# Kernel optimization log

Measured on AMD Instinct MI355X. Metric: run time of the kernel, lower is better.

Reference implementation:

```python
import jax, jax.numpy as jnp
import numpy as np

Q, C, S, D = 2048, 10, 16, 256
H = [256, 128, 64, 10]

def _init_linear(key, fan_in, fan_out):
    kw, kb = jax.random.split(key)
    bound = 1.0 / np.sqrt(fan_in)
    W = jax.random.uniform(kw, (fan_in, fan_out), jnp.float32, -bound, bound)
    b = jax.random.uniform(kb, (fan_out,), jnp.float32, -bound, bound)
    return W, b

def setup_inputs() -> dict:
    key = jax.random.key(0)
    ks = jax.random.split(key, 6)
    queries = jax.random.normal(ks[0], (Q, D), jnp.float32)
    supports = jax.random.normal(ks[1], (C, S, D), jnp.float32)
    W1, b1 = _init_linear(ks[2], 2 * D, H[0])
    W2, b2 = _init_linear(ks[3], H[0], H[1])
    W3, b3 = _init_linear(ks[4], H[1], H[2])
    W4, b4 = _init_linear(ks[5], H[2], H[3])
    return {"queries": queries, "supports": supports,
            "W1": W1, "b1": b1, "W2": W2, "b2": b2,
            "W3": W3, "b3": b3, "W4": W4, "b4": b4}

def reference(queries, supports, W1, b1, W2, b2, W3, b3, W4, b4):
    # queries: [Q, D]; supports: [C, S, D]
    q, d = queries.shape
    c, s, _ = supports.shape
    # Build all (query, support-item) pairs: [Q, C, S, 2D]
    qb = jnp.broadcast_to(queries[:, None, None, :], (q, c, s, d))
    sb = jnp.broadcast_to(supports[None, :, :, :], (q, c, s, d))
    x = jnp.concatenate([qb, sb], axis=-1)
    h = jax.nn.relu(x @ W1 + b1)
    h = jax.nn.relu(h @ W2 + b2)
    h = jax.nn.relu(h @ W3 + b3)
    out = jnp.tanh(h @ W4 + b4)          # [Q, C, S, 10]
    item_score = out.mean(axis=-1)       # [Q, C, S] (Simnet mean over 10 outputs)
    scores = item_score.sum(axis=-1)     # sum over support items -> [Q, C]
    return scores
```

## Files before the change

kernel.cpp:

```cpp
#include <hip/hip_runtime.h>
#include <hip/hip_bf16.h>
#include <math.h>

#define QN 2048
#define CN 10
#define SN 16
#define DN 256
#define H1N 256
#define H2N 128
#define H3N 64
#define H4N 10
#define NROW 160
#define PRE_AB_BLOCKS (QN / 4 + NROW / 4)

#define S1 528
#define S2 272
#define S3 144

typedef __attribute__((ext_vector_type(8)))  short  bf16x8s;
typedef __attribute__((ext_vector_type(4)))  float  f32x4;
typedef __attribute__((ext_vector_type(16))) float  f32x16;

static __device__ __forceinline__ unsigned short f2bf(float f) {
  __hip_bfloat16 h = __float2bfloat16(f);
  return __builtin_bit_cast(unsigned short, h);
}

static __device__ __forceinline__ float fast_tanh(float x) {
  const float xc = fminf(fmaxf(x, -15.f), 15.f);
  const float e = __expf(2.f * xc);
  return (e - 1.f) / (e + 1.f);
}

__global__ __launch_bounds__(256) void k_pre(
    const float* __restrict__ queries, const float* __restrict__ supports,
    const float* __restrict__ W1, const float* __restrict__ b1,
    const float* __restrict__ W2, const float* __restrict__ W3,
    const float* __restrict__ W4,
    float* __restrict__ A, float* __restrict__ Bm,
    ushort* __restrict__ fb2, ushort* __restrict__ fb3, ushort* __restrict__ fb4) {
  __shared__ float xs[4][DN];
  const int bid = blockIdx.x;
  const int t = threadIdx.x;

  if (bid < PRE_AB_BLOCKS) {
    const bool isA = bid < (QN / 4);
    const int row0 = isA ? bid * 4 : (bid - QN / 4) * 4;
    const float* src = isA ? (queries + (size_t)row0 * DN) : (supports + (size_t)row0 * DN);
    for (int r = 0; r < 4; ++r) xs[r][t] = src[r * DN + t];
    __syncthreads();
    const float* w = W1 + (isA ? 0 : DN * H1N) + t;
    float acc0 = 0.f, acc1 = 0.f, acc2 = 0.f, acc3 = 0.f;
#pragma unroll 8
    for (int d = 0; d < DN; ++d) {
      const float wv = w[(size_t)d * H1N];
      acc0 += xs[0][d] * wv;
      acc1 += xs[1][d] * wv;
      acc2 += xs[2][d] * wv;
      acc3 += xs[3][d] * wv;
    }
    const float bias = isA ? b1[t] : 0.f;
    float* dst = isA ? A : Bm;
    dst[(row0 + 0) * H1N + t] = acc0 + bias;
    dst[(row0 + 1) * H1N + t] = acc1 + bias;
    dst[(row0 + 2) * H1N + t] = acc2 + bias;
    dst[(row0 + 3) * H1N + t] = acc3 + bias;
    return;
  }

  const int f = (bid - PRE_AB_BLOCKS) * 4 + (t >> 6);
  const int l = t & 63;
  if (f >= 82) return;
  ushort o[8];
  if (f < 64) {
    const int ct = f >> 4, ks = f & 15;
    const int col = ct * 32 + (l & 31);
    const int k0 = ks * 16 + (l >> 5) * 8;
#pragma unroll
    for (int j = 0; j < 8; ++j) o[j] = f2bf(W2[(size_t)(k0 + j) * H2N + col]);
#pragma unroll
    for (int j = 0; j < 8; ++j) fb2[(size_t)f * 512 + l * 8 + j] = o[j];
  } else if (f < 80) {
    const int g = f - 64;
    const int ct = g >> 3, ks = g & 7;
    const int col = ct * 32 + (l & 31);
    const int k0 = ks * 16 + (l >> 5) * 8;
#pragma unroll
    for (int j = 0; j < 8; ++j) o[j] = f2bf(W3[(size_t)(k0 + j) * H3N + col]);
#pragma unroll
    for (int j = 0; j < 8; ++j) fb3[(size_t)g * 512 + l * 8 + j] = o[j];
  } else {
    const int ks = f - 80;
    const int col = l & 15;
    const int k0 = ks * 32 + (l >> 4) * 8;
#pragma unroll
    for (int j = 0; j < 8; ++j)
      o[j] = (col < H4N) ? f2bf(W4[(size_t)(k0 + j) * H4N + col]) : (ushort)0;
#pragma unroll
    for (int j = 0; j < 8; ++j) fb4[(size_t)ks * 512 + l * 8 + j] = o[j];
  }
}

__global__ __launch_bounds__(512, 2) void k_main(
    const float* __restrict__ A, const float* __restrict__ Bm,
    const ushort* __restrict__ fb2, const ushort* __restrict__ fb3,
    const ushort* __restrict__ fb4,
    const float* __restrict__ b2, const float* __restrict__ b3,
    const float* __restrict__ b4, float* __restrict__ out) {
  __shared__ __align__(16) unsigned char smem[128 * S1];
  unsigned char* h1s = smem;
  unsigned char* h2s = smem;
  unsigned char* h3s = smem + 128 * S2;

  const int t = threadIdx.x;
  const int wid = t >> 6;
  const int l = t & 63;
  const int l31 = l & 31;
  const int l15 = l & 15;
  const int wr = wid >> 1;
  const int wc = wid & 1;

  const bf16x8s* fb2v = (const bf16x8s*)fb2;
  const bf16x8s* fb3v = (const bf16x8s*)fb3;
  const bf16x8s* fb4v = (const bf16x8s*)fb4;

  bf16x8s B3r[8];
#pragma unroll
  for (int ks = 0; ks < 8; ++ks) B3r[ks] = fb3v[(wc * 8 + ks) * 64 + l];
  const int c0g2 = 64 * wc + l31;
  const float bias2a = b2[c0g2], bias2b = b2[c0g2 + 32];
  const float bias3 = b3[32 * wc + l31];

  const int rg0 = blockIdx.x * 128;
  const int q0 = rg0 / NROW;
  const int b0 = rg0 - q0 * NROW;
#pragma unroll 4
  for (int r = 0; r < 16; ++r) {
    const int row = wid * 16 + r;
    int bb = b0 + row;
    int qq = q0;
    if (bb >= NROW) { bb -= NROW; qq += 1; }
    const float4 av = *(const float4*)(A + (size_t)qq * DN + l * 4);
    const float4 bv = *(const float4*)(Bm + (size_t)bb * DN + l * 4);
    ushort4 o;
    o.x = f2bf(fmaxf(av.x + bv.x, 0.f));
    o.y = f2bf(fmaxf(av.y + bv.y, 0.f));
    o.z = f2bf(fmaxf(av.z + bv.z, 0.f));
    o.w = f2bf(fmaxf(av.w + bv.w, 0.f));
    *(ushort4*)(h1s + row * S1 + l * 8) = o;
  }
  __syncthreads();

  f32x16 acc2a, acc2b;
#pragma unroll
  for (int i = 0; i < 16; ++i) { acc2a[i] = 0.f; acc2b[i] = 0.f; }
  {
    const unsigned char* abase = h1s + (32 * wr + l31) * S1;
    const int kh = (l >> 5) * 16;
    const int ct0 = wc * 2;
    bf16x8s a_cur = *(const bf16x8s*)(abase + kh);
    bf16x8s pA0 = fb2v[((ct0 + 0) * 16 + 0) * 64 + l];
    bf16x8s pB0 = fb2v[((ct0 + 1) * 16 + 0) * 64 + l];
    bf16x8s pA1 = fb2v[((ct0 + 0) * 16 + 1) * 64 + l];
    bf16x8s pB1 = fb2v[((ct0 + 1) * 16 + 1) * 64 + l];
#pragma unroll
    for (int ks = 0; ks < 16; ++ks) {
      const bf16x8s a_use = a_cur;
      const bf16x8s bA = (ks & 1) ? pA1 : pA0;
      const bf16x8s bB = (ks & 1) ? pB1 : pB0;
      if (ks + 1 < 16) a_cur = *(const bf16x8s*)(abase + (ks + 1) * 32 + kh);
      if (ks + 2 < 16) {
        if (ks & 1) {
          pA1 = fb2v[((ct0 + 0) * 16 + ks + 2) * 64 + l];
          pB1 = fb2v[((ct0 + 1) * 16 + ks + 2) * 64 + l];
        } else {
          pA0 = fb2v[((ct0 + 0) * 16 + ks + 2) * 64 + l];
          pB0 = fb2v[((ct0 + 1) * 16 + ks + 2) * 64 + l];
        }
      }
      acc2a = __builtin_amdgcn_mfma_f32_32x32x16_bf16(a_use, bA, acc2a, 0, 0, 0);
      acc2b = __builtin_amdgcn_mfma_f32_32x32x16_bf16(a_use, bB, acc2b, 0, 0, 0);
    }
  }
  __syncthreads();
  {
#pragma unroll
    for (int reg = 0; reg < 16; ++reg) {
      const int row = 32 * wr + (reg & 3) + 8 * (reg >> 2) + 4 * (l >> 5);
      *(ushort*)(h2s + row * S2 + c0g2 * 2) =
          f2bf(fmaxf(acc2a[reg] + bias2a, 0.f));
      *(ushort*)(h2s + row * S2 + c0g2 * 2 + 64) =
          f2bf(fmaxf(acc2b[reg] + bias2b, 0.f));
    }
  }

  bf16x8s B4r[2];
  B4r[0] = fb4v[l];
  B4r[1] = fb4v[64 + l];
  const float b4v = (l15 < H4N) ? b4[l15] : 0.f;
  __syncthreads();

  f32x16 acc3;
#pragma unroll
  for (int i = 0; i < 16; ++i) acc3[i] = 0.f;
  {
    const unsigned char* abase = h2s + (32 * wr + l31) * S2;
    const int kh = (l >> 5) * 16;
    bf16x8s a_cur = *(const bf16x8s*)(abase + kh);
#pragma unroll
    for (int ks = 0; ks < 8; ++ks) {
      const bf16x8s a_use = a_cur;
      if (ks + 1 < 8) a_cur = *(const bf16x8s*)(abase + (ks + 1) * 32 + kh);
      acc3 = __builtin_amdgcn_mfma_f32_32x32x16_bf16(a_use, B3r[ks], acc3, 0, 0, 0);
    }
  }
  {
#pragma unroll
    for (int reg = 0; reg < 16; ++reg) {
      const int row = 32 * wr + (reg & 3) + 8 * (reg >> 2) + 4 * (l >> 5);
      *(ushort*)(h3s + row * S3 + (32 * wc + l31) * 2) =
          f2bf(fmaxf(acc3[reg] + bias3, 0.f));
    }
  }
  __syncthreads();

  f32x4 acc4;
#pragma unroll
  for (int i = 0; i < 4; ++i) acc4[i] = 0.f;
  {
    const unsigned char* abase = h3s + (16 * wid + l15) * S3;
#pragma unroll
    for (int ks = 0; ks < 2; ++ks) {
      const bf16x8s a = *(const bf16x8s*)(abase + (l >> 4) * 16 + ks * 64);
      acc4 = __builtin_amdgcn_mfma_f32_16x16x32_bf16(a, B4r[ks], acc4, 0, 0, 0);
    }
  }

  {
    float part = 0.f;
#pragma unroll
    for (int r = 0; r < 4; ++r) {
      const float v = fast_tanh(acc4[r] + b4v);
      part += (l15 < H4N) ? v : 0.f;
    }
    part += __shfl_xor(part, 1);
    part += __shfl_xor(part, 2);
    part += __shfl_xor(part, 4);
    part += __shfl_xor(part, 8);
    part += __shfl_xor(part, 16);
    part += __shfl_xor(part, 32);
    if (l == 0) out[(size_t)blockIdx.x * 8 + wid] = part * 0.1f;
  }
}

extern "C" void kernel_launch(void* const* d_in, const int* in_sizes, int n_in,
                              void* d_out, int out_size, void* d_ws, size_t ws_size,
                              hipStream_t stream) {
  const float* queries  = (const float*)d_in[0];
  const float* supports = (const float*)d_in[1];
  const float* W1 = (const float*)d_in[2];
  const float* b1 = (const float*)d_in[3];
  const float* W2 = (const float*)d_in[4];
  const float* b2 = (const float*)d_in[5];
  const float* W3 = (const float*)d_in[6];
  const float* b3 = (const float*)d_in[7];
  const float* W4 = (const float*)d_in[8];
  const float* b4 = (const float*)d_in[9];
  float* out = (float*)d_out;

  float* A  = (float*)d_ws;
  float* Bm = A + (size_t)QN * H1N;
  ushort* fb2 = (ushort*)(Bm + (size_t)NROW * H1N);
  ushort* fb3 = fb2 + 64 * 512;
  ushort* fb4 = fb3 + 16 * 512;

  hipLaunchKernelGGL(k_pre, dim3(PRE_AB_BLOCKS + 21), dim3(256), 0, stream,
                     queries, supports, W1, b1, W2, W3, W4, A, Bm, fb2, fb3, fb4);
  hipLaunchKernelGGL(k_main, dim3((QN * CN * SN) / 128), dim3(512), 0, stream,
                     A, Bm, fb2, fb3, fb4, b2, b3, b4, out);
}
```

Before: 74.68 us.

## Split layer-2 K into halves to shrink LDS and raise occupancy

The layer-1 activation tile is now built and consumed in two K-halves of 128 columns through a smaller shared buffer, so LDS per block drops from about 66KB to about 53KB. The launch bound is raised from 2 to 6 blocks per multiprocessor. Manual software prefetching of A and B fragments is removed in favour of direct loads. The goal is to hide latency through higher occupancy, at the cost of extra barriers, register pressure from the tighter launch bound, and less explicit overlap within each wave.

```diff
diff --git a/kernel.cpp b/kernel.cpp
--- a/kernel.cpp
+++ b/kernel.cpp
@@ -13,8 +13,7 @@
 #define NROW 160
 #define PRE_AB_BLOCKS (QN / 4 + NROW / 4)
 
-#define S1 528
-#define S2 272
+#define SH 272
 #define S3 144
 
 typedef __attribute__((ext_vector_type(8)))  short  bf16x8s;
@@ -101,22 +100,23 @@
   }
 }
 
-__global__ __launch_bounds__(512, 2) void k_main(
+__global__ __launch_bounds__(512, 6) void k_main(
     const float* __restrict__ A, const float* __restrict__ Bm,
     const ushort* __restrict__ fb2, const ushort* __restrict__ fb3,
     const ushort* __restrict__ fb4,
     const float* __restrict__ b2, const float* __restrict__ b3,
     const float* __restrict__ b4, float* __restrict__ out) {
-  __shared__ __align__(16) unsigned char smem[128 * S1];
+  __shared__ __align__(16) unsigned char smem[128 * SH + 128 * S3];
   unsigned char* h1s = smem;
   unsigned char* h2s = smem;
-  unsigned char* h3s = smem + 128 * S2;
+  unsigned char* h3s = smem + 128 * SH;
 
   const int t = threadIdx.x;
   const int wid = t >> 6;
   const int l = t & 63;
   const int l31 = l & 31;
   const int l15 = l & 15;
+  const int lh = l >> 5;
   const int wr = wid >> 1;
   const int wc = wid & 1;
 
@@ -134,62 +134,53 @@
   const int rg0 = blockIdx.x * 128;
   const int q0 = rg0 / NROW;
   const int b0 = rg0 - q0 * NROW;
-#pragma unroll 4
-  for (int r = 0; r < 16; ++r) {
-    const int row = wid * 16 + r;
-    int bb = b0 + row;
-    int qq = q0;
-    if (bb >= NROW) { bb -= NROW; qq += 1; }
-    const float4 av = *(const float4*)(A + (size_t)qq * DN + l * 4);
-    const float4 bv = *(const float4*)(Bm + (size_t)bb * DN + l * 4);
-    ushort4 o;
-    o.x = f2bf(fmaxf(av.x + bv.x, 0.f));
-    o.y = f2bf(fmaxf(av.y + bv.y, 0.f));
-    o.z = f2bf(fmaxf(av.z + bv.z, 0.f));
-    o.w = f2bf(fmaxf(av.w + bv.w, 0.f));
-    *(ushort4*)(h1s + row * S1 + l * 8) = o;
-  }
-  __syncthreads();
+  const int ct0 = wc * 2;
+  const unsigned char* abase2 = h1s + (32 * wr + l31) * SH;
+  const int kh = lh * 16;
 
   f32x16 acc2a, acc2b;
 #pragma unroll
   for (int i = 0; i < 16; ++i) { acc2a[i] = 0.f; acc2b[i] = 0.f; }
-  {
-    const unsigned char* abase = h1s + (32 * wr + l31) * S1;
-    const int kh = (l >> 5) * 16;
-    const int ct0 = wc * 2;
-    bf16x8s a_cur = *(const bf16x8s*)(abase + kh);
-    bf16x8s pA0 = fb2v[((ct0 + 0) * 16 + 0) * 64 + l];
-    bf16x8s pB0 = fb2v[((ct0 + 1) * 16 + 0) * 64 + l];
-    bf16x8s pA1 = fb2v[((ct0 + 0) * 16 + 1) * 64 + l];
-    bf16x8s pB1 = fb2v[((ct0 + 1) * 16 + 1) * 64 + l];
-#pragma unroll
-    for (int ks = 0; ks < 16; ++ks) {
-      const bf16x8s a_use = a_cur;
-      const bf16x8s bA = (ks & 1) ? pA1 : pA0;
-      const bf16x8s bB = (ks & 1) ? pB1 : pB0;
-      if (ks + 1 < 16) a_cur = *(const bf16x8s*)(abase + (ks + 1) * 32 + kh);
-      if (ks + 2 < 16) {
-        if (ks & 1) {
-          pA1 = fb2v[((ct0 + 0) * 16 + ks + 2) * 64 + l];
-          pB1 = fb2v[((ct0 + 1) * 16 + ks + 2) * 64 + l];
-        } else {
-          pA0 = fb2v[((ct0 + 0) * 16 + ks + 2) * 64 + l];
-          pB0 = fb2v[((ct0 + 1) * 16 + ks + 2) * 64 + l];
-        }
-      }
-      acc2a = __builtin_amdgcn_mfma_f32_32x32x16_bf16(a_use, bA, acc2a, 0, 0, 0);
-      acc2b = __builtin_amdgcn_mfma_f32_32x32x16_bf16(a_use, bB, acc2b, 0, 0, 0);
-    }
-  }
-  __syncthreads();
+
+#pragma unroll
+  for (int hf = 0; hf < 2; ++hf) {
+#pragma unroll
+    for (int it = 0; it < 8; ++it) {
+      const int row = wid * 16 + it * 2 + lh;
+      int bb = b0 + row;
+      int qq = q0;
+      if (bb >= NROW) { bb -= NROW; qq += 1; }
+      const int col = hf * 128 + l31 * 4;
+      const float4 av = *(const float4*)(A + (size_t)qq * DN + col);
+      const float4 bv = *(const float4*)(Bm + (size_t)bb * DN + col);
+      ushort4 o;
+      o.x = f2bf(fmaxf(av.x + bv.x, 0.f));
+      o.y = f2bf(fmaxf(av.y + bv.y, 0.f));
+      o.z = f2bf(fmaxf(av.z + bv.z, 0.f));
+      o.w = f2bf(fmaxf(av.w + bv.w, 0.f));
+      *(ushort4*)(h1s + row * SH + l31 * 8) = o;
+    }
+    __syncthreads();
+
+#pragma unroll
+    for (int ks = 0; ks < 8; ++ks) {
+      const int ksg = hf * 8 + ks;
+      const bf16x8s a = *(const bf16x8s*)(abase2 + ks * 32 + kh);
+      const bf16x8s bA = fb2v[((ct0 + 0) * 16 + ksg) * 64 + l];
+      const bf16x8s bB = fb2v[((ct0 + 1) * 16 + ksg) * 64 + l];
+      acc2a = __builtin_amdgcn_mfma_f32_32x32x16_bf16(a, bA, acc2a, 0, 0, 0);
+      acc2b = __builtin_amdgcn_mfma_f32_32x32x16_bf16(a, bB, acc2b, 0, 0, 0);
+    }
+    __syncthreads();
+  }
+
   {
 #pragma unroll
     for (int reg = 0; reg < 16; ++reg) {
-      const int row = 32 * wr + (reg & 3) + 8 * (reg >> 2) + 4 * (l >> 5);
-      *(ushort*)(h2s + row * S2 + c0g2 * 2) =
+      const int row = 32 * wr + (reg & 3) + 8 * (reg >> 2) + 4 * lh;
+      *(ushort*)(h2s + row * SH + c0g2 * 2) =
           f2bf(fmaxf(acc2a[reg] + bias2a, 0.f));
-      *(ushort*)(h2s + row * S2 + c0g2 * 2 + 64) =
+      *(ushort*)(h2s + row * SH + c0g2 * 2 + 64) =
           f2bf(fmaxf(acc2b[reg] + bias2b, 0.f));
     }
   }
@@ -204,20 +195,17 @@
 #pragma unroll
   for (int i = 0; i < 16; ++i) acc3[i] = 0.f;
   {
-    const unsigned char* abase = h2s + (32 * wr + l31) * S2;
-    const int kh = (l >> 5) * 16;
-    bf16x8s a_cur = *(const bf16x8s*)(abase + kh);
+    const unsigned char* abase = h2s + (32 * wr + l31) * SH;
 #pragma unroll
     for (int ks = 0; ks < 8; ++ks) {
-      const bf16x8s a_use = a_cur;
-      if (ks + 1 < 8) a_cur = *(const bf16x8s*)(abase + (ks + 1) * 32 + kh);
-      acc3 = __builtin_amdgcn_mfma_f32_32x32x16_bf16(a_use, B3r[ks], acc3, 0, 0, 0);
+      const bf16x8s a = *(const bf16x8s*)(abase + ks * 32 + kh);
+      acc3 = __builtin_amdgcn_mfma_f32_32x32x16_bf16(a, B3r[ks], acc3, 0, 0, 0);
     }
   }
   {
 #pragma unroll
     for (int reg = 0; reg < 16; ++reg) {
-      const int row = 32 * wr + (reg & 3) + 8 * (reg >> 2) + 4 * (l >> 5);
+      const int row = 32 * wr + (reg & 3) + 8 * (reg >> 2) + 4 * lh;
       *(ushort*)(h3s + row * S3 + (32 * wc + l31) * 2) =
           f2bf(fmaxf(acc3[reg] + bias3, 0.f));
     }
```

New measurement: 141.6 us. 89.6% more time.
